# Kernel optimization log

Hardware: AMD Instinct MI355X
Metric: run time of the kernel (lower is better)

The kernel has to match this reference:

```python
import jax, jax.numpy as jnp
import numpy as np

NUM_GRAPHS = 1024
NODES_PER_GRAPH = 128
NUM_EDGES = 1048576
D_IN = 128          # n_heads * head_out_feats = input/concat dim
ATT_HEADS = 2       # intra/inter GATConv(d, 32, 2) as in HDN-DDI repo
ATT_OUT = 32
POOL_HEADS = 2      # pool = GATConv(128, 64, 2)
POOL_OUT = 64
EPS = 1e-5          # PyG LayerNorm eps


def _segment_softmax(e, seg, n):
    # numerically-stable softmax over edges grouped by destination node
    m = jax.ops.segment_max(e, seg, num_segments=n)
    m = jnp.where(jnp.isfinite(m), m, 0.0)
    p = jnp.exp(e - m[seg])
    s = jax.ops.segment_sum(p, seg, num_segments=n)
    return p / (s[seg] + 1e-16)


def _gat(x_src, x_dst, edge_index, w_src, w_dst, att_src, att_dst, bias, self_loops):
    # PyG GATConv: linear -> per-head attention logits -> leaky_relu(0.2) ->
    # softmax over incoming edges -> weighted sum of source features -> concat heads + bias
    H, C = att_src.shape
    nd = x_dst.shape[0]
    hs = (x_src @ w_src).reshape(-1, H, C)   # [Ns,H,C]
    hd = (x_dst @ w_dst).reshape(-1, H, C)   # [Nd,H,C]
    a_s = jnp.einsum('nhc,hc->nh', hs, att_src)
    a_d = jnp.einsum('nhc,hc->nh', hd, att_dst)
    src, dst = edge_index[0], edge_index[1]
    if self_loops:  # PyG default add_self_loops=True (non-bipartite case)
        loop = jnp.arange(nd)
        src = jnp.concatenate([src, loop])
        dst = jnp.concatenate([dst, loop])
    e = jax.nn.leaky_relu(a_s[src] + a_d[dst], 0.2)  # [E,H]
    alpha = _segment_softmax(e, dst, nd)
    out = jax.ops.segment_sum(hs[src] * alpha[:, :, None], dst, num_segments=nd)
    return out.reshape(nd, H * C) + bias


def _graph_layernorm(x, batch, weight, bias, n_graphs):
    # PyG LayerNorm(mode='graph'): normalize over all nodes+channels of each graph
    f = x.shape[-1]
    cnt = jax.ops.segment_sum(jnp.ones((x.shape[0],), x.dtype), batch, num_segments=n_graphs)
    norm = jnp.maximum(cnt, 1.0) * f
    mean = jax.ops.segment_sum(x.sum(-1), batch, num_segments=n_graphs) / norm
    xc = x - mean[batch][:, None]
    var = jax.ops.segment_sum((xc * xc).sum(-1), batch, num_segments=n_graphs) / norm
    return (xc / jnp.sqrt(var + EPS)[batch][:, None]) * weight + bias


def setup_inputs() -> dict:
    key = jax.random.key(0)
    ks = jax.random.split(key, 24)
    B, P, E, D = NUM_GRAPHS, NODES_PER_GRAPH, NUM_EDGES, D_IN
    N = B * P

    def intra_edges(k):  # within-graph edges, no self-loops
        k1, k2, k3 = jax.random.split(k, 3)
        g = jax.random.randint(k1, (E,), 0, B)
        s = jax.random.randint(k2, (E,), 0, P)
        d = (s + 1 + jax.random.randint(k3, (E,), 0, P - 1)) % P
        return jnp.stack([g * P + s, g * P + d])

    def inter_edges(k):  # bipartite head-node -> tail-node edges within same graph pair
        k1, k2, k3 = jax.random.split(k, 3)
        g = jax.random.randint(k1, (E,), 0, B)
        s = jax.random.randint(k2, (E,), 0, P)
        d = jax.random.randint(k3, (E,), 0, P)
        return jnp.stack([g * P + s, g * P + d])

    batch = jnp.repeat(jnp.arange(B), P)
    # one global supernode (type 2) per graph: the last node
    y = jnp.tile(jnp.concatenate([jnp.zeros((P - 1,), jnp.int32), jnp.array([2], jnp.int32)]), B)
    p = lambda k, shape: jax.random.normal(k, shape, jnp.float32) * 0.1
    return {
        'h_x': jax.random.normal(ks[0], (N, D), jnp.float32),
        't_x': jax.random.normal(ks[1], (N, D), jnp.float32),
        'h_edge_index': intra_edges(ks[2]),
        't_edge_index': intra_edges(ks[3]),
        'b_edge_index': inter_edges(ks[4]),
        'h_batch': batch,
        't_batch': batch,
        'h_y': y,
        't_y': y,
        'w_intra': p(ks[5], (D, ATT_HEADS * ATT_OUT)),
        'att_intra_src': p(ks[6], (ATT_HEADS, ATT_OUT)),
        'att_intra_dst': p(ks[7], (ATT_HEADS, ATT_OUT)),
        'b_intra': jnp.zeros((ATT_HEADS * ATT_OUT,), jnp.float32),
        'w_inter_src': p(ks[8], (D, ATT_HEADS * ATT_OUT)),
        'w_inter_dst': p(ks[9], (D, ATT_HEADS * ATT_OUT)),
        'att_inter_src': p(ks[10], (ATT_HEADS, ATT_OUT)),
        'att_inter_dst': p(ks[11], (ATT_HEADS, ATT_OUT)),
        'b_inter': jnp.zeros((ATT_HEADS * ATT_OUT,), jnp.float32),
        'w_pool': p(ks[12], (D, POOL_HEADS * POOL_OUT)),
        'att_pool_src': p(ks[13], (POOL_HEADS, POOL_OUT)),
        'att_pool_dst': p(ks[14], (POOL_HEADS, POOL_OUT)),
        'b_pool': jnp.zeros((POOL_HEADS * POOL_OUT,), jnp.float32),
        'ln_weight': jnp.ones((D,), jnp.float32),
        'ln_bias': jnp.zeros((D,), jnp.float32),
    }


def reference(h_x, t_x, h_edge_index, t_edge_index, b_edge_index, h_batch, t_batch, h_y, t_y,
              w_intra, att_intra_src, att_intra_dst, b_intra,
              w_inter_src, w_inter_dst, att_inter_src, att_inter_dst, b_inter,
              w_pool, att_pool_src, att_pool_dst, b_pool, ln_weight, ln_bias):
    h_in = jax.nn.elu(h_x)
    t_in = jax.nn.elu(t_x)
    # intra-graph attention (shared GATConv applied to both drug graphs)
    h_intra = _gat(h_in, h_in, h_edge_index, w_intra, w_intra, att_intra_src, att_intra_dst, b_intra, True)
    t_intra = _gat(t_in, t_in, t_edge_index, w_intra, w_intra, att_intra_src, att_intra_dst, b_intra, True)
    # inter-graph (bipartite) attention: h->t and reversed t->h with shared weights
    t_inter = _gat(h_in, t_in, b_edge_index, w_inter_src, w_inter_dst, att_inter_src, att_inter_dst, b_inter, False)
    h_inter = _gat(t_in, h_in, b_edge_index[::-1], w_inter_src, w_inter_dst, att_inter_src, att_inter_dst, b_inter, False)
    h_rep = jnp.concatenate([h_intra, h_inter], 1)  # [N, 128]
    t_rep = jnp.concatenate([t_intra, t_inter], 1)
    h_nx = jax.nn.elu(_graph_layernorm(h_rep, h_batch, ln_weight, ln_bias, NUM_GRAPHS))
    t_nx = jax.nn.elu(_graph_layernorm(t_rep, t_batch, ln_weight, ln_bias, NUM_GRAPHS))
    h_out = _gat(h_nx, h_nx, h_edge_index, w_pool, w_pool, att_pool_src, att_pool_dst, b_pool, True)
    t_out = _gat(t_nx, t_nx, t_edge_index, w_pool, w_pool, att_pool_src, att_pool_dst, b_pool, True)
    # get_node: gather the single type-2 supernode per graph (exactly NUM_GRAPHS of them)
    h_idx = jnp.where(h_y == 2, size=NUM_GRAPHS)[0]
    t_idx = jnp.where(t_y == 2, size=NUM_GRAPHS)[0]
    return h_out, t_out, h_out[h_idx], t_out[t_idx]
```

## Files before the change

kernel.cpp:

```cpp
#include <hip/hip_runtime.h>
#include <hip/hip_bf16.h>

#define NN 131072
#define NG 1024
#define NE 1048576
#define EB 16384
#define NB 64
#define EMAX 1536

typedef __hip_bfloat16 bf16;
typedef __attribute__((ext_vector_type(8))) short short8v;
typedef __attribute__((ext_vector_type(4))) float f32x4;

__device__ __forceinline__ float b2f(bf16 v){ return __bfloat162float(v); }
__device__ __forceinline__ bf16 f2b(float v){ return __float2bfloat16(v); }
__device__ __forceinline__ unsigned short f2bu(float v){ bf16 b = f2b(v); return *(unsigned short*)&b; }
__device__ __forceinline__ float eluf(float x){ return x > 0.f ? x : expm1f(x); }
__device__ __forceinline__ float lrelu(float x){ return x >= 0.f ? x : 0.2f*x; }

__device__ __forceinline__ float ldx(const void* p, size_t i, int f){
  return f ? ((const float*)p)[i] : b2f(((const bf16*)p)[i]);
}

struct EPtrs { const int *s0,*d0,*s1,*d1,*s2,*d2,*s3,*d3; };

__global__ void detect_dtype(const unsigned short* __restrict__ x, int* __restrict__ flag){
  if (blockIdx.x==0 && threadIdx.x==0){
    int bad = 0;
    for (int i=0;i<2048;i++){
      unsigned short e = (x[i] >> 7) & 0xFF;
      if (e == 0xFF) bad++;
      else if (e >= 0x90) bad++;
      else if (e != 0 && e < 0x60) bad++;
    }
    *flag = (bad > 64) ? 1 : 0;
  }
}

__global__ __launch_bounds__(256) void hist_bagg(EPtrs ep, int* __restrict__ Hb){
  __shared__ int cnt[NG];
  int set = blockIdx.y, blk = blockIdx.x, t = threadIdx.x;
  const int* dp = set==0 ? ep.d0 : set==1 ? ep.d1 : set==2 ? ep.d2 : ep.d3;
  for (int i=t;i<NG;i+=256) cnt[i]=0;
  __syncthreads();
  int e0 = blk*EB;
  for (int i=t;i<EB;i+=256) atomicAdd(&cnt[dp[e0+i]>>7],1);
  __syncthreads();
  for (int i=t;i<NG;i+=256) Hb[((size_t)set*NB+blk)*NG+i] = cnt[i];
}

__global__ __launch_bounds__(1024) void scan_bagg(const int* __restrict__ Hb, int* __restrict__ Bb,
                                                  int* __restrict__ base_gs){
  __shared__ int sh[1024];
  int set = blockIdx.x, t = threadIdx.x;
  int run = 0;
  for (int b=0;b<NB;b++){
    int v = Hb[((size_t)set*NB + b)*NG + t];
    Bb[((size_t)set*NB + b)*NG + t] = run;
    run += v;
  }
  int val = run; sh[t] = run; __syncthreads();
  for (int d=1; d<1024; d<<=1){
    int add = (t>=d)? sh[t-d] : 0; __syncthreads();
    val += add; sh[t] = val; __syncthreads();
  }
  int binbase = val - run;
  base_gs[set*(NG+1) + t] = binbase;
  if (t==1023) base_gs[set*(NG+1)+NG] = val;
  for (int b=0;b<NB;b++) Bb[((size_t)set*NB + b)*NG + t] += binbase;
}

__global__ __launch_bounds__(256) void scatter_bagg(EPtrs ep, const int* __restrict__ Bb,
                                                    unsigned short* __restrict__ pk){
  __shared__ int cur[NG];
  int set = blockIdx.y, blk = blockIdx.x, t = threadIdx.x;
  const int* sp = set==0 ? ep.s0 : set==1 ? ep.s1 : set==2 ? ep.s2 : ep.s3;
  const int* dp = set==0 ? ep.d0 : set==1 ? ep.d1 : set==2 ? ep.d2 : ep.d3;
  for (int i=t;i<NG;i+=256) cur[i] = Bb[((size_t)set*NB+blk)*NG+i];
  __syncthreads();
  int e0 = blk*EB;
  for (int i=t;i<EB;i+=256){
    int e = e0+i;
    int d = dp[e], s = sp[e];
    int p = atomicAdd(&cur[d>>7],1);
    pk[(size_t)set*NE + p] = (unsigned short)(((d & 127) << 8) | (s & 127));
  }
}

__global__ __launch_bounds__(256) void build_csr(const unsigned short* __restrict__ pk, const int* __restrict__ base,
                                                 unsigned char* __restrict__ srcs8, int* __restrict__ offs4){
  __shared__ int hist[128], excl[128], cur[128];
  __shared__ unsigned char ob[8192];
  int set = blockIdx.y, g = blockIdx.x, t = threadIdx.x;
  int n0 = base[set*(NG+1) + g], n1 = base[set*(NG+1) + g + 1];
  int cnt = min(n1 - n0, 8192);
  if (t < 128) hist[t] = 0;
  __syncthreads();
  const unsigned short* PK = pk + (size_t)set*NE + n0;
  for (int i=t; i<cnt; i+=256) atomicAdd(&hist[PK[i]>>8], 1);
  __syncthreads();
  if (t < 128) excl[t] = hist[t];
  __syncthreads();
  for (int d=1; d<128; d<<=1){
    int v = (t < 128 && t >= d) ? excl[t-d] : 0;
    __syncthreads();
    if (t < 128) excl[t] += v;
    __syncthreads();
  }
  if (t < 128){
    int e_ = excl[t] - hist[t];
    cur[t] = e_;
    offs4[(size_t)set*(NN+1) + g*128 + t] = n0 + e_;
  }
  if (g == NG-1 && t == 0) offs4[(size_t)set*(NN+1) + NN] = NE;
  __syncthreads();
  for (int i=t; i<cnt; i+=256){
    unsigned short v = PK[i];
    int p = atomicAdd(&cur[v>>8], 1);
    ob[p] = (unsigned char)(v & 127);
  }
  __syncthreads();
  unsigned char* S = srcs8 + (size_t)set*NE + n0;
  for (int i=t; i<cnt; i+=256) S[i] = ob[i];
}

__global__ __launch_bounds__(256) void prep_kernel(
    const void* w_intra, const void* w_isrc, const void* w_idst, const void* att_xd, const void* w_pool,
    const void* att_is, const void* att_id, const void* att_xs,
    const void* att_ps, const void* att_pd,
    const void* b_intra, const void* b_inter, const void* b_pool,
    const void* ln_w, const void* ln_b,
    bf16* __restrict__ Wtc, bf16* __restrict__ Wtp, float* __restrict__ vdst, float* __restrict__ sm,
    const int* __restrict__ fp){
  int f = *fp;
  int t = threadIdx.x;
  for (int i=t; i<16384; i+=256){
    int j = i & 7, l = (i>>3) & 63, ks = (i>>9) & 3, nt = i >> 11;
    int k = ks*32 + ((l>>4)<<3) + j;
    int c = nt*16 + (l & 15);
    float w1 = (c < 64) ? ldx(w_intra, k*64 + c, f) : ldx(w_isrc, k*64 + (c-64), f);
    Wtc[i] = f2b(w1);
    Wtp[i] = f2b(ldx(w_pool, k*128 + c, f));
  }
  {
    int k = t>>1, h = t&1; float a = 0.f;
    for (int c=0;c<32;c++) a += ldx(w_idst, k*64 + h*32 + c, f) * ldx(att_xd, h*32 + c, f);
    vdst[t] = a;
  }
  if (t < 64){
    sm[t]     = ldx(att_is, t, f);
    sm[64+t]  = ldx(att_id, t, f);
    sm[128+t] = ldx(att_xs, t, f);
    sm[448+t] = ldx(b_intra, t, f);
    sm[512+t] = ldx(b_inter, t, f);
  }
  if (t < 128){
    sm[192+t] = ldx(att_ps, t, f);
    sm[320+t] = ldx(att_pd, t, f);
    sm[576+t] = ldx(b_pool, t, f);
    sm[704+t] = ldx(ln_w, t, f);
    sm[832+t] = ldx(ln_b, t, f);
  }
}

template<int MODE>
__global__ __launch_bounds__(256) void gemm_fused(const void* A, const bf16* __restrict__ Wt, bf16* __restrict__ C,
    const int* __restrict__ fp, const int* __restrict__ fsel, size_t aoff_bf, size_t aoff_f32,
    const float* __restrict__ vdst,
    const float* __restrict__ attA, const float* __restrict__ attB, const float* __restrict__ attC,
    float* __restrict__ oS, float* __restrict__ oD, float* __restrict__ oX, float* __restrict__ oDx){
  constexpr bool ELU = (MODE==0);
  const bf16* Ab = (const bf16*)A + ((fp == nullptr && fsel && *fsel) ? aoff_f32 : aoff_bf);
  int tid = threadIdx.x;
  int w = tid >> 6, l = tid & 63;
  int lr = l & 15, lg = l >> 4;
  size_t row = (size_t)blockIdx.x*64 + w*16 + lr;
  int f = fp ? *fp : 0;
  f32x4 acc[8];
  #pragma unroll
  for (int nt=0;nt<8;nt++) acc[nt] = (f32x4){0.f,0.f,0.f,0.f};
  float dx0 = 0.f, dx1 = 0.f;
  #pragma unroll
  for (int ks=0;ks<4;ks++){
    short8v af;
    size_t ab = row*128 + ks*32 + lg*8;
    if (fp){
      if (f){
        const float* Af = (const float*)A;
        #pragma unroll
        for (int j=0;j<8;j++){
          float v = Af[ab+j]; if (ELU) v = eluf(v);
          if constexpr (MODE==0){ int k = ks*32+lg*8+j; dx0 += v*vdst[k*2]; dx1 += v*vdst[k*2+1]; }
          ((unsigned short*)&af)[j] = f2bu(v);
        }
      } else {
        const unsigned short* Au = (const unsigned short*)A;
        short8v raw = *(const short8v*)(Au + ab);
        #pragma unroll
        for (int j=0;j<8;j++){
          bf16 b; *(unsigned short*)&b = ((unsigned short*)&raw)[j];
          float v = b2f(b); if (ELU) v = eluf(v);
          if constexpr (MODE==0){ int k = ks*32+lg*8+j; dx0 += v*vdst[k*2]; dx1 += v*vdst[k*2+1]; }
          ((unsigned short*)&af)[j] = f2bu(v);
        }
      }
    } else {
      af = *(const short8v*)((const unsigned short*)Ab + ab);
    }
    #pragma unroll
    for (int nt=0;nt<8;nt++){
      short8v bfr = *(const short8v*)((const unsigned short*)Wt + (size_t)((nt*4+ks)*64 + l)*8);
      acc[nt] = __builtin_amdgcn_mfma_f32_16x16x32_bf16(af, bfr, acc[nt], 0, 0, 0);
    }
  }
  if constexpr (MODE==0){
    dx0 += __shfl_xor(dx0, 16); dx0 += __shfl_xor(dx0, 32);
    dx1 += __shfl_xor(dx1, 16); dx1 += __shfl_xor(dx1, 32);
    if (lg == 0){ oDx[row*2] = dx0; oDx[row*2+1] = dx1; }
  }
  size_t crow = (size_t)blockIdx.x*64 + w*16 + lg*4;
  #pragma unroll
  for (int nt=0;nt<8;nt++)
    #pragma unroll
    for (int r=0;r<4;r++)
      C[(crow + r)*128 + nt*16 + lr] = f2b(acc[nt][r]);
  #pragma unroll
  for (int rg=0; rg<4; ++rg){
    float pS0=0.f,pS1=0.f,pD0=0.f,pD1=0.f,pX0=0.f,pX1=0.f;
    #pragma unroll
    for (int nt=0;nt<8;nt++){
      float v = acc[nt][rg];
      int c = nt*16 + lr;
      if constexpr (MODE==0){
        if (nt<4){
          float a=attA[c], b=attB[c];
          if (nt<2){ pS0+=v*a; pD0+=v*b; } else { pS1+=v*a; pD1+=v*b; }
        } else {
          float xw=attC[c-64];
          if (nt<6) pX0+=v*xw; else pX1+=v*xw;
        }
      } else {
        float a=attA[c], b=attB[c];
        if (nt<4){ pS0+=v*a; pD0+=v*b; } else { pS1+=v*a; pD1+=v*b; }
      }
    }
    #pragma unroll
    for (int o=1;o<16;o<<=1){
      pS0+=__shfl_xor(pS0,o); pS1+=__shfl_xor(pS1,o);
      pD0+=__shfl_xor(pD0,o); pD1+=__shfl_xor(pD1,o);
      if constexpr (MODE==0){ pX0+=__shfl_xor(pX0,o); pX1+=__shfl_xor(pX1,o); }
    }
    if (lr == 0){
      size_t n = crow + rg;
      oS[n*2]=pS0; oS[n*2+1]=pS1;
      oD[n*2]=pD0; oD[n*2+1]=pD1;
      if constexpr (MODE==0){ oX[n*2]=pX0; oX[n*2+1]=pX1; }
    }
  }
}

struct GatSet {
  const int* offs;
  const unsigned char* srcs;
  const bf16* F;
  const float* aS;
  const float* aD;
  const float* bias;
  int col_in;
  int self_loops;
  int col_off;
  int pad;
  size_t obase_bf, obase_f32, gbase;
};
struct GatSet4 { GatSet s[4]; };

template<int FD>
__global__ __launch_bounds__(512) void gat_mfma(GatSet4 sets, void* out,
    const int* __restrict__ fp, const int* __restrict__ fsel){
  constexpr int NH = FD/2;
  constexpr int NT = NH/16;
  constexpr int KSH = (FD==64)?5:6;
  __shared__ bf16 Ft[NH*136];
  __shared__ bf16 Pm[128*136];
  __shared__ float2 aSs[128];
  __shared__ float rsum[128];
  __shared__ unsigned char ss[EMAX];
  __shared__ int begs[129];
  const GatSet S = sets.s[blockIdx.y];
  int fo = fp ? *fp : -1;
  size_t obase = (fsel && *fsel) ? S.obase_f32 : S.obase_bf;
  int g = blockIdx.x, t = threadIdx.x;

  if (t < 129) begs[t] = S.offs[g*128 + t];
  if (t >= 256 && t < 384) aSs[t-256] = ((const float2*)S.aS)[g*128 + (t-256)];
  __syncthreads();
  int gbeg = begs[0];
  int Eg = min(begs[128] - gbeg, EMAX);
  int w = t >> 6, l = t & 63, lr = l & 15, lg = l >> 4;

  #pragma unroll
  for (int h=0; h<2; ++h){
    for (int i=t; i<128*68; i+=512) ((unsigned int*)Pm)[i] = 0;
    if (h==0) for (int i=t; i<Eg; i+=512) ss[i] = S.srcs[gbeg + i];
    __syncthreads();
    if (t < 128){
      int r = t;
      float ad = S.aD[(size_t)(g*128+r)*2 + h];
      int b = begs[r]-gbeg, e = min(begs[r+1]-gbeg, EMAX);
      float rs = 0.f;
      unsigned short* Pr = (unsigned short*)Pm + r*136;
      for (int j=b; j<e; ++j){
        int s = ss[j];
        float2 as2 = aSs[s];
        float p = __expf(lrelu((h ? as2.y : as2.x) + ad));
        bf16 ov; *(unsigned short*)&ov = Pr[s];
        Pr[s] = f2bu(b2f(ov) + p);
        rs += p;
      }
      if (S.self_loops){
        float2 as2 = aSs[r];
        float p = __expf(lrelu((h ? as2.y : as2.x) + ad));
        bf16 ov; *(unsigned short*)&ov = Pr[r];
        Pr[r] = f2bu(b2f(ov) + p);
        rs += p;
      }
      rsum[r] = rs;
    } else {
      const unsigned short* Fu = (const unsigned short*)S.F;
      unsigned short* FtU = (unsigned short*)Ft;
      int ft = t - 128;
      for (int i=ft; i<NH*128; i+=384){
        int c = i & (NH-1), k = i >> KSH;
        FtU[c*136 + k] = Fu[((size_t)(g*128+k))*128 + S.col_in + h*NH + c];
      }
    }
    __syncthreads();
    f32x4 acc[NT];
    #pragma unroll
    for (int nt=0;nt<NT;nt++) acc[nt] = (f32x4){0.f,0.f,0.f,0.f};
    #pragma unroll
    for (int ks=0;ks<4;ks++){
      short8v af = *(const short8v*)((const unsigned short*)Pm + (w*16+lr)*136 + ks*32 + lg*8);
      #pragma unroll
      for (int nt=0;nt<NT;nt++){
        short8v bfr = *(const short8v*)((const unsigned short*)Ft + (nt*16 + lr)*136 + ks*32 + lg*8);
        acc[nt] = __builtin_amdgcn_mfma_f32_16x16x32_bf16(af, bfr, acc[nt], 0, 0, 0);
      }
    }
    #pragma unroll
    for (int rg=0; rg<4; ++rg){
      int rrow = w*16 + lg*4 + rg;
      float rinv = 1.f / (rsum[rrow] + 1e-16f);
      int n = g*128 + rrow;
      bool gw = (fp != nullptr) && (rrow == 127);
      #pragma unroll
      for (int nt=0;nt<NT;nt++){
        int c = h*NH + nt*16 + lr;
        float o = acc[nt][rg]*rinv + S.bias[c];
        size_t oi = obase + (size_t)n*128 + S.col_off + c;
        if (fo > 0){
          ((float*)out)[oi] = o;
          if (gw) ((float*)out)[S.gbase + (size_t)g*128 + c] = o;
        } else {
          ((bf16*)out)[oi] = f2b(o);
          if (gw) ((bf16*)out)[S.gbase + (size_t)g*128 + c] = f2b(o);
        }
      }
    }
    __syncthreads();
  }
}

__global__ __launch_bounds__(512) void graph_ln_m(bf16* R_, size_t off_t_bf, size_t off_t_f32,
    const int* __restrict__ fsel, const float* __restrict__ wv, const float* __restrict__ bv){
  __shared__ float sh1[8], sh2[8];
  int g = blockIdx.x, t = threadIdx.x;
  int side = g >> 10, gl = g & 1023;
  size_t soff = side ? ((*fsel) ? off_t_f32 : off_t_bf) : 0;
  unsigned short* Ru = (unsigned short*)(R_ + soff + (size_t)gl*16384);
  short8v v[4];
  #pragma unroll
  for (int q=0;q<4;q++) v[q] = *(short8v*)(Ru + q*4096 + t*8);
  float s1=0.f, s2=0.f;
  #pragma unroll
  for (int q=0;q<4;q++)
    #pragma unroll
    for (int j=0;j<8;j++){
      bf16 b; *(unsigned short*)&b = ((unsigned short*)&v[q])[j];
      float x = b2f(b); s1 += x; s2 += x*x;
    }
  #pragma unroll
  for (int o=32;o;o>>=1){ s1 += __shfl_xor(s1,o); s2 += __shfl_xor(s2,o); }
  if ((t&63)==0){ sh1[t>>6]=s1; sh2[t>>6]=s2; }
  __syncthreads();
  float S1=0.f,S2=0.f;
  #pragma unroll
  for (int i=0;i<8;i++){ S1+=sh1[i]; S2+=sh2[i]; }
  float mean = S1 * (1.f/16384.f);
  float var = fmaxf(S2*(1.f/16384.f) - mean*mean, 0.f);
  float rstd = rsqrtf(var + 1e-5f);
  #pragma unroll
  for (int q=0;q<4;q++){
    short8v ov;
    #pragma unroll
    for (int j=0;j<8;j++){
      int c = (t*8 + j) & 127;
      bf16 b; *(unsigned short*)&b = ((unsigned short*)&v[q])[j];
      float y = (b2f(b)-mean)*rstd*wv[c] + bv[c];
      ((unsigned short*)&ov)[j] = f2bu(y>0.f ? y : expm1f(y));
    }
    *(short8v*)(Ru + q*4096 + t*8) = ov;
  }
}

extern "C" void kernel_launch(void* const* d_in, const int* in_sizes, int n_in,
                              void* d_out, int out_size, void* d_ws, size_t ws_size,
                              hipStream_t stream){
  (void)in_sizes; (void)n_in; (void)out_size; (void)ws_size;
  const void* h_x = d_in[0];
  const void* t_x = d_in[1];
  const int* h_ei = (const int*)d_in[2];
  const int* t_ei = (const int*)d_in[3];
  const int* b_ei = (const int*)d_in[4];

  char* base = (char*)d_ws;
  size_t off = 0;
  auto alloc = [&](size_t bytes)->char*{ char* p = base + off; off += (bytes + 255) & ~(size_t)255; return p; };
  bf16* AB_h     = (bf16*)alloc((size_t)NN*128*2);
  bf16* AB_t     = (bf16*)alloc((size_t)NN*128*2);
  unsigned short* pk = (unsigned short*)alloc((size_t)4*NE*2);
  unsigned char* srcs8 = (unsigned char*)alloc((size_t)4*NE);
  int* offs4     = (int*)alloc((size_t)4*(NN+1)*4);
  int* Hb        = (int*)alloc((size_t)4*NB*NG*4);
  int* Bb        = (int*)alloc((size_t)4*NB*NG*4);
  int* base_gs   = (int*)alloc((size_t)4*(NG+1)*4);
  float* aSi_h   = (float*)alloc((size_t)NN*2*4);
  float* aDi_h   = (float*)alloc((size_t)NN*2*4);
  float* aSx_h   = (float*)alloc((size_t)NN*2*4);
  float* aSi_t   = (float*)alloc((size_t)NN*2*4);
  float* aDi_t   = (float*)alloc((size_t)NN*2*4);
  float* aSx_t   = (float*)alloc((size_t)NN*2*4);
  float* aDx_h   = (float*)alloc((size_t)NN*2*4);
  float* aDx_t   = (float*)alloc((size_t)NN*2*4);
  bf16* Wtc      = (bf16*)alloc(16384*2);
  bf16* Wtp      = (bf16*)alloc(16384*2);
  float* vdst    = (float*)alloc(256*4);
  float* sm      = (float*)alloc(960*4);
  int* flag      = (int*)alloc(256);

  const size_t REPT_BF = (size_t)NN*128, REPT_F32 = (size_t)2*NN*128;

  detect_dtype<<<1,64,0,stream>>>((const unsigned short*)h_x, flag);

  EPtrs ep;
  ep.s0 = h_ei;      ep.d0 = h_ei + NE;
  ep.s1 = t_ei;      ep.d1 = t_ei + NE;
  ep.s2 = b_ei;      ep.d2 = b_ei + NE;
  ep.s3 = b_ei + NE; ep.d3 = b_ei;
  hist_bagg<<<dim3(NB,4),256,0,stream>>>(ep, Hb);
  scan_bagg<<<4,1024,0,stream>>>(Hb, Bb, base_gs);
  scatter_bagg<<<dim3(NB,4),256,0,stream>>>(ep, Bb, pk);
  build_csr<<<dim3(NG,4),256,0,stream>>>(pk, base_gs, srcs8, offs4);

  prep_kernel<<<1,256,0,stream>>>(d_in[9], d_in[13], d_in[14], d_in[16], d_in[18],
      d_in[10], d_in[11], d_in[15], d_in[19], d_in[20],
      d_in[12], d_in[17], d_in[21], d_in[22], d_in[23],
      Wtc, Wtp, vdst, sm, flag);

  const int* offs_h = offs4;
  const int* offs_t = offs4 + (NN+1);
  const int* offs_ht= offs4 + 2*(NN+1);
  const int* offs_th= offs4 + 3*(NN+1);
  const unsigned char* srcs_h = srcs8;
  const unsigned char* srcs_t = srcs8 + NE;
  const unsigned char* srcs_ht= srcs8 + (size_t)2*NE;
  const unsigned char* srcs_th= srcs8 + (size_t)3*NE;

  gemm_fused<0><<<2048,256,0,stream>>>(h_x, Wtc, AB_h, flag, nullptr, 0, 0,
      vdst, sm+0, sm+64, sm+128, aSi_h, aDi_h, aSx_h, aDx_h);
  gemm_fused<0><<<2048,256,0,stream>>>(t_x, Wtc, AB_t, flag, nullptr, 0, 0,
      vdst, sm+0, sm+64, sm+128, aSi_t, aDi_t, aSx_t, aDx_t);

  {
    GatSet4 L;
    L.s[0] = { offs_h,  srcs_h,  AB_h, aSi_h, aDi_h, sm+448, 0,  1, 0,  0, 0,        0,         0 };
    L.s[1] = { offs_t,  srcs_t,  AB_t, aSi_t, aDi_t, sm+448, 0,  1, 0,  0, REPT_BF,  REPT_F32,  0 };
    L.s[2] = { offs_ht, srcs_ht, AB_h, aSx_h, aDx_t, sm+512, 64, 0, 64, 0, REPT_BF,  REPT_F32,  0 };
    L.s[3] = { offs_th, srcs_th, AB_t, aSx_t, aDx_h, sm+512, 64, 0, 64, 0, 0,        0,         0 };
    gat_mfma<64><<<dim3(NG,4),512,0,stream>>>(L, d_out, nullptr, flag);
  }

  graph_ln_m<<<2048,512,0,stream>>>((bf16*)d_out, REPT_BF, REPT_F32, flag, sm+704, sm+832);

  gemm_fused<1><<<2048,256,0,stream>>>(d_out, Wtp, AB_h, nullptr, flag, 0, 0,
      nullptr, sm+192, sm+320, nullptr, aSi_h, aDi_h, nullptr, nullptr);
  gemm_fused<1><<<2048,256,0,stream>>>(d_out, Wtp, AB_t, nullptr, flag, REPT_BF, REPT_F32,
      nullptr, sm+192, sm+320, nullptr, aSi_t, aDi_t, nullptr, nullptr);

  {
    size_t gb_h = (size_t)2*NN*128;
    size_t gb_t = gb_h + (size_t)NG*128;
    GatSet4 P;
    P.s[0] = { offs_h, srcs_h, AB_h, aSi_h, aDi_h, sm+576, 0, 1, 0, 0, 0,              0,              gb_h };
    P.s[1] = { offs_t, srcs_t, AB_t, aSi_t, aDi_t, sm+576, 0, 1, 0, 0, (size_t)NN*128, (size_t)NN*128, gb_t };
    P.s[2] = P.s[0]; P.s[3] = P.s[0];
    gat_mfma<128><<<dim3(NG,2),512,0,stream>>>(P, d_out, flag, flag);
  }
}
```

Measured before the change: 615.5 us.

## Fuse node projection GEMMs into per-graph GAT kernels and drop intermediates

Removes the standalone projection GEMM kernels and instead computes the linear projections and attention logits inside each per-graph GAT block, keeping the projected features in registers and shared memory rather than writing them to global memory and reading them back. The layer-norm intermediate now lives in a bf16 workspace, so the LN kernel no longer branches on dtype. A small separate kernel precomputes the bipartite destination logits. In exchange, each inter-graph set recomputes its half of the projection, the weights are staged into shared memory per block, and shared memory per block grows, which may lower occupancy.

Result: faster. 585.4 us (-4.9%).

```diff
diff --git a/kernel.cpp b/kernel.cpp
--- a/kernel.cpp
+++ b/kernel.cpp
@@ -163,207 +163,320 @@
   }
 }
 
-template<int MODE>
-__global__ __launch_bounds__(256) void gemm_fused(const void* A, const bf16* __restrict__ Wt, bf16* __restrict__ C,
-    const int* __restrict__ fp, const int* __restrict__ fsel, size_t aoff_bf, size_t aoff_f32,
-    const float* __restrict__ vdst,
-    const float* __restrict__ attA, const float* __restrict__ attB, const float* __restrict__ attC,
-    float* __restrict__ oS, float* __restrict__ oD, float* __restrict__ oX, float* __restrict__ oDx){
-  constexpr bool ELU = (MODE==0);
-  const bf16* Ab = (const bf16*)A + ((fp == nullptr && fsel && *fsel) ? aoff_f32 : aoff_bf);
-  int tid = threadIdx.x;
-  int w = tid >> 6, l = tid & 63;
-  int lr = l & 15, lg = l >> 4;
-  size_t row = (size_t)blockIdx.x*64 + w*16 + lr;
-  int f = fp ? *fp : 0;
-  f32x4 acc[8];
-  #pragma unroll
-  for (int nt=0;nt<8;nt++) acc[nt] = (f32x4){0.f,0.f,0.f,0.f};
-  float dx0 = 0.f, dx1 = 0.f;
+__global__ __launch_bounds__(256) void avec_dx_m(const void* Xh, const void* Xt, const float* __restrict__ vdst,
+                                                 float* __restrict__ aDx_h, float* __restrict__ aDx_t,
+                                                 const int* __restrict__ fp){
+  int f = *fp;
+  int gid = blockIdx.x*256 + threadIdx.x;
+  int n = gid >> 6, lane = gid & 63;
+  int side = n >= NN;
+  const void* X = side ? Xt : Xh;
+  float* aDx = side ? aDx_t : aDx_h;
+  int nl = side ? n - NN : n;
+  float x1 = eluf(ldx(X, (size_t)nl*128 + lane, f));
+  float x2 = eluf(ldx(X, (size_t)nl*128 + 64 + lane, f));
+  float t0 = x1*vdst[lane*2+0] + x2*vdst[(lane+64)*2+0];
+  float t1 = x1*vdst[lane*2+1] + x2*vdst[(lane+64)*2+1];
+  #pragma unroll
+  for (int o=32;o;o>>=1){ t0 += __shfl_xor(t0,o); t1 += __shfl_xor(t1,o); }
+  if (lane == 0){ aDx[nl*2+0] = t0; aDx[nl*2+1] = t1; }
+}
+
+struct L1Set {
+  const int* offs;
+  const unsigned char* srcs;
+  int a_side;
+  int wt_half;
+  int att_mode;
+  int col_off;
+  const float* aDx;
+  bf16* repout;
+};
+struct L1Set4 { L1Set s[4]; };
+
+__global__ __launch_bounds__(512) void gat_l1(L1Set4 sets, const void* Xh, const void* Xt,
+    const bf16* __restrict__ Wtc, const float* __restrict__ sm, const int* __restrict__ fp){
+  __shared__ char U[34816];
+  __shared__ bf16 Ft[32*136];
+  __shared__ float atab[192];
+  __shared__ float2 aSl[128], aDl[128];
+  __shared__ float rsum[128];
+  __shared__ unsigned char ss[EMAX];
+  __shared__ int begs[129];
+  const L1Set S = sets.s[blockIdx.y];
+  int g = blockIdx.x, t = threadIdx.x;
+  int f = *fp;
+  const void* A = S.a_side ? Xt : Xh;
+
+  bf16* WtL = (bf16*)U;
+  {
+    const short8v* src = (const short8v*)(Wtc + (size_t)S.wt_half*8192);
+    short8v* dst = (short8v*)WtL;
+    #pragma unroll
+    for (int i=0;i<2;i++) dst[t + i*512] = src[t + i*512];
+  }
+  if (t < 129) begs[t] = S.offs[g*128 + t];
+  if (t < 192){
+    float v;
+    if (t < 64) v = sm[(S.att_mode ? 128 : 0) + t];
+    else if (t < 128) v = sm[64 + (t-64)];
+    else v = sm[(S.att_mode ? 512 : 448) + (t-128)];
+    atab[t] = v;
+  }
+  __syncthreads();
+  int gbeg = begs[0], Eg = min(begs[128]-gbeg, EMAX);
+  for (int i=t; i<Eg; i+=512) ss[i] = S.srcs[gbeg + i];
+
+  int w = t>>6, l = t&63, lr = l&15, lg = l>>4;
+  size_t row = (size_t)g*128 + w*16 + lr;
+  f32x4 acc[4];
+  #pragma unroll
+  for (int nt=0;nt<4;nt++) acc[nt] = (f32x4){0.f,0.f,0.f,0.f};
   #pragma unroll
   for (int ks=0;ks<4;ks++){
     short8v af;
     size_t ab = row*128 + ks*32 + lg*8;
-    if (fp){
-      if (f){
-        const float* Af = (const float*)A;
-        #pragma unroll
-        for (int j=0;j<8;j++){
-          float v = Af[ab+j]; if (ELU) v = eluf(v);
-          if constexpr (MODE==0){ int k = ks*32+lg*8+j; dx0 += v*vdst[k*2]; dx1 += v*vdst[k*2+1]; }
-          ((unsigned short*)&af)[j] = f2bu(v);
-        }
-      } else {
-        const unsigned short* Au = (const unsigned short*)A;
-        short8v raw = *(const short8v*)(Au + ab);
-        #pragma unroll
-        for (int j=0;j<8;j++){
-          bf16 b; *(unsigned short*)&b = ((unsigned short*)&raw)[j];
-          float v = b2f(b); if (ELU) v = eluf(v);
-          if constexpr (MODE==0){ int k = ks*32+lg*8+j; dx0 += v*vdst[k*2]; dx1 += v*vdst[k*2+1]; }
-          ((unsigned short*)&af)[j] = f2bu(v);
-        }
-      }
+    if (f){
+      const float* Af = (const float*)A;
+      #pragma unroll
+      for (int j=0;j<8;j++){ ((unsigned short*)&af)[j] = f2bu(eluf(Af[ab+j])); }
     } else {
-      af = *(const short8v*)((const unsigned short*)Ab + ab);
-    }
-    #pragma unroll
-    for (int nt=0;nt<8;nt++){
-      short8v bfr = *(const short8v*)((const unsigned short*)Wt + (size_t)((nt*4+ks)*64 + l)*8);
+      const unsigned short* Au = (const unsigned short*)A;
+      short8v raw = *(const short8v*)(Au + ab);
+      #pragma unroll
+      for (int j=0;j<8;j++){
+        bf16 b; *(unsigned short*)&b = ((unsigned short*)&raw)[j];
+        ((unsigned short*)&af)[j] = f2bu(eluf(b2f(b)));
+      }
+    }
+    #pragma unroll
+    for (int nt=0;nt<4;nt++){
+      short8v bfr = *(const short8v*)((const unsigned short*)WtL + (size_t)((nt*4+ks)*64 + l)*8);
       acc[nt] = __builtin_amdgcn_mfma_f32_16x16x32_bf16(af, bfr, acc[nt], 0, 0, 0);
     }
   }
-  if constexpr (MODE==0){
-    dx0 += __shfl_xor(dx0, 16); dx0 += __shfl_xor(dx0, 32);
-    dx1 += __shfl_xor(dx1, 16); dx1 += __shfl_xor(dx1, 32);
-    if (lg == 0){ oDx[row*2] = dx0; oDx[row*2+1] = dx1; }
-  }
-  size_t crow = (size_t)blockIdx.x*64 + w*16 + lg*4;
-  #pragma unroll
-  for (int nt=0;nt<8;nt++)
-    #pragma unroll
-    for (int r=0;r<4;r++)
-      C[(crow + r)*128 + nt*16 + lr] = f2b(acc[nt][r]);
   #pragma unroll
   for (int rg=0; rg<4; ++rg){
-    float pS0=0.f,pS1=0.f,pD0=0.f,pD1=0.f,pX0=0.f,pX1=0.f;
-    #pragma unroll
-    for (int nt=0;nt<8;nt++){
+    float pS0=0.f,pS1=0.f,pD0=0.f,pD1=0.f;
+    #pragma unroll
+    for (int nt=0;nt<4;nt++){
       float v = acc[nt][rg];
       int c = nt*16 + lr;
-      if constexpr (MODE==0){
-        if (nt<4){
-          float a=attA[c], b=attB[c];
-          if (nt<2){ pS0+=v*a; pD0+=v*b; } else { pS1+=v*a; pD1+=v*b; }
-        } else {
-          float xw=attC[c-64];
-          if (nt<6) pX0+=v*xw; else pX1+=v*xw;
-        }
-      } else {
-        float a=attA[c], b=attB[c];
-        if (nt<4){ pS0+=v*a; pD0+=v*b; } else { pS1+=v*a; pD1+=v*b; }
-      }
+      float a = atab[c], b = atab[64+c];
+      if (nt<2){ pS0 += v*a; pD0 += v*b; } else { pS1 += v*a; pD1 += v*b; }
     }
     #pragma unroll
     for (int o=1;o<16;o<<=1){
       pS0+=__shfl_xor(pS0,o); pS1+=__shfl_xor(pS1,o);
       pD0+=__shfl_xor(pD0,o); pD1+=__shfl_xor(pD1,o);
-      if constexpr (MODE==0){ pX0+=__shfl_xor(pX0,o); pX1+=__shfl_xor(pX1,o); }
     }
     if (lr == 0){
-      size_t n = crow + rg;
-      oS[n*2]=pS0; oS[n*2+1]=pS1;
-      oD[n*2]=pD0; oD[n*2+1]=pD1;
-      if constexpr (MODE==0){ oX[n*2]=pX0; oX[n*2+1]=pX1; }
-    }
-  }
-}
-
-struct GatSet {
-  const int* offs;
-  const unsigned char* srcs;
-  const bf16* F;
-  const float* aS;
-  const float* aD;
-  const float* bias;
-  int col_in;
-  int self_loops;
-  int col_off;
-  int pad;
-  size_t obase_bf, obase_f32, gbase;
-};
-struct GatSet4 { GatSet s[4]; };
-
-template<int FD>
-__global__ __launch_bounds__(512) void gat_mfma(GatSet4 sets, void* out,
-    const int* __restrict__ fp, const int* __restrict__ fsel){
-  constexpr int NH = FD/2;
-  constexpr int NT = NH/16;
-  constexpr int KSH = (FD==64)?5:6;
-  __shared__ bf16 Ft[NH*136];
-  __shared__ bf16 Pm[128*136];
-  __shared__ float2 aSs[128];
-  __shared__ float rsum[128];
-  __shared__ unsigned char ss[EMAX];
-  __shared__ int begs[129];
-  const GatSet S = sets.s[blockIdx.y];
-  int fo = fp ? *fp : -1;
-  size_t obase = (fsel && *fsel) ? S.obase_f32 : S.obase_bf;
-  int g = blockIdx.x, t = threadIdx.x;
-
-  if (t < 129) begs[t] = S.offs[g*128 + t];
-  if (t >= 256 && t < 384) aSs[t-256] = ((const float2*)S.aS)[g*128 + (t-256)];
-  __syncthreads();
-  int gbeg = begs[0];
-  int Eg = min(begs[128] - gbeg, EMAX);
-  int w = t >> 6, l = t & 63, lr = l & 15, lg = l >> 4;
-
+      int rr = w*16 + lg*4 + rg;
+      aSl[rr] = make_float2(pS0, pS1);
+      if (S.att_mode == 0) aDl[rr] = make_float2(pD0, pD1);
+    }
+  }
+  if (S.att_mode == 1 && t < 128) aDl[t] = ((const float2*)S.aDx)[g*128 + t];
+  __syncthreads();
+
+  bf16* Pm = (bf16*)U;
   #pragma unroll
   for (int h=0; h<2; ++h){
     for (int i=t; i<128*68; i+=512) ((unsigned int*)Pm)[i] = 0;
-    if (h==0) for (int i=t; i<Eg; i+=512) ss[i] = S.srcs[gbeg + i];
+    #pragma unroll
+    for (int ntl=0; ntl<2; ++ntl){
+      int nt = h*2 + ntl;
+      #pragma unroll
+      for (int rg=0; rg<4; ++rg)
+        ((unsigned short*)Ft)[(ntl*16+lr)*136 + (w*16+lg*4+rg)] = f2bu(acc[nt][rg]);
+    }
     __syncthreads();
     if (t < 128){
       int r = t;
-      float ad = S.aD[(size_t)(g*128+r)*2 + h];
+      float ad = h ? aDl[r].y : aDl[r].x;
       int b = begs[r]-gbeg, e = min(begs[r+1]-gbeg, EMAX);
       float rs = 0.f;
       unsigned short* Pr = (unsigned short*)Pm + r*136;
       for (int j=b; j<e; ++j){
         int s = ss[j];
-        float2 as2 = aSs[s];
-        float p = __expf(lrelu((h ? as2.y : as2.x) + ad));
+        float as = h ? aSl[s].y : aSl[s].x;
+        float p = __expf(lrelu(as + ad));
         bf16 ov; *(unsigned short*)&ov = Pr[s];
         Pr[s] = f2bu(b2f(ov) + p);
         rs += p;
       }
-      if (S.self_loops){
-        float2 as2 = aSs[r];
-        float p = __expf(lrelu((h ? as2.y : as2.x) + ad));
+      if (S.att_mode == 0){
+        float as = h ? aSl[r].y : aSl[r].x;
+        float p = __expf(lrelu(as + ad));
         bf16 ov; *(unsigned short*)&ov = Pr[r];
         Pr[r] = f2bu(b2f(ov) + p);
         rs += p;
       }
       rsum[r] = rs;
-    } else {
-      const unsigned short* Fu = (const unsigned short*)S.F;
-      unsigned short* FtU = (unsigned short*)Ft;
-      int ft = t - 128;
-      for (int i=ft; i<NH*128; i+=384){
-        int c = i & (NH-1), k = i >> KSH;
-        FtU[c*136 + k] = Fu[((size_t)(g*128+k))*128 + S.col_in + h*NH + c];
-      }
-    }
-    __syncthreads();
-    f32x4 acc[NT];
-    #pragma unroll
-    for (int nt=0;nt<NT;nt++) acc[nt] = (f32x4){0.f,0.f,0.f,0.f};
+    }
+    __syncthreads();
+    f32x4 a2[2];
+    a2[0] = (f32x4){0.f,0.f,0.f,0.f}; a2[1] = (f32x4){0.f,0.f,0.f,0.f};
     #pragma unroll
     for (int ks=0;ks<4;ks++){
       short8v af = *(const short8v*)((const unsigned short*)Pm + (w*16+lr)*136 + ks*32 + lg*8);
       #pragma unroll
-      for (int nt=0;nt<NT;nt++){
-        short8v bfr = *(const short8v*)((const unsigned short*)Ft + (nt*16 + lr)*136 + ks*32 + lg*8);
-        acc[nt] = __builtin_amdgcn_mfma_f32_16x16x32_bf16(af, bfr, acc[nt], 0, 0, 0);
+      for (int j=0;j<2;j++){
+        short8v bfr = *(const short8v*)((const unsigned short*)Ft + (j*16+lr)*136 + ks*32 + lg*8);
+        a2[j] = __builtin_amdgcn_mfma_f32_16x16x32_bf16(af, bfr, a2[j], 0, 0, 0);
       }
     }
     #pragma unroll
     for (int rg=0; rg<4; ++rg){
       int rrow = w*16 + lg*4 + rg;
       float rinv = 1.f / (rsum[rrow] + 1e-16f);
-      int n = g*128 + rrow;
-      bool gw = (fp != nullptr) && (rrow == 127);
-      #pragma unroll
-      for (int nt=0;nt<NT;nt++){
-        int c = h*NH + nt*16 + lr;
-        float o = acc[nt][rg]*rinv + S.bias[c];
-        size_t oi = obase + (size_t)n*128 + S.col_off + c;
-        if (fo > 0){
+      size_t n = (size_t)g*128 + rrow;
+      #pragma unroll
+      for (int j=0;j<2;j++){
+        int c = h*32 + j*16 + lr;
+        float o = a2[j][rg]*rinv + atab[128+c];
+        S.repout[n*128 + S.col_off + c] = f2b(o);
+      }
+    }
+    __syncthreads();
+  }
+}
+
+__global__ __launch_bounds__(512) void gat_pool(const bf16* __restrict__ rep,
+    const int* __restrict__ offs_h, const unsigned char* __restrict__ srcs_h,
+    const int* __restrict__ offs_t, const unsigned char* __restrict__ srcs_t,
+    const bf16* __restrict__ Wtp, const float* __restrict__ sm,
+    void* out, const int* __restrict__ fp){
+  __shared__ char U[34816];
+  __shared__ bf16 Ft[64*136];
+  __shared__ float attL[384];
+  __shared__ float2 aSp[128], aDp[128];
+  __shared__ float rsum[128];
+  __shared__ unsigned char ss[EMAX];
+  __shared__ int begs[129];
+  int side = blockIdx.y, g = blockIdx.x, t = threadIdx.x;
+  int f = *fp;
+  const int* offs = side ? offs_t : offs_h;
+  const unsigned char* srcs = side ? srcs_t : srcs_h;
+  const unsigned short* A = (const unsigned short*)rep + (size_t)side*NN*128;
+  size_t obase = (size_t)side*NN*128;
+  size_t gbase = (size_t)2*NN*128 + (size_t)side*NG*128;
+
+  bf16* WtL = (bf16*)U;
+  {
+    const short8v* src = (const short8v*)Wtp;
+    short8v* dst = (short8v*)WtL;
+    #pragma unroll
+    for (int i=0;i<4;i++) dst[t + i*512] = src[t + i*512];
+  }
+  if (t < 129) begs[t] = offs[g*128 + t];
+  if (t < 384) attL[t] = sm[(t<128) ? 192+t : (t<256) ? 320+(t-128) : 576+(t-256)];
+  __syncthreads();
+  int gbeg = begs[0], Eg = min(begs[128]-gbeg, EMAX);
+  for (int i=t; i<Eg; i+=512) ss[i] = srcs[gbeg + i];
+
+  int w = t>>6, l = t&63, lr = l&15, lg = l>>4;
+  size_t row = (size_t)g*128 + w*16 + lr;
+  f32x4 acc[8];
+  #pragma unroll
+  for (int nt=0;nt<8;nt++) acc[nt] = (f32x4){0.f,0.f,0.f,0.f};
+  #pragma unroll
+  for (int ks=0;ks<4;ks++){
+    short8v af = *(const short8v*)(A + row*128 + ks*32 + lg*8);
+    #pragma unroll
+    for (int nt=0;nt<8;nt++){
+      short8v bfr = *(const short8v*)((const unsigned short*)WtL + (size_t)((nt*4+ks)*64 + l)*8);
+      acc[nt] = __builtin_amdgcn_mfma_f32_16x16x32_bf16(af, bfr, acc[nt], 0, 0, 0);
+    }
+  }
+  #pragma unroll
+  for (int rg=0; rg<4; ++rg){
+    float pS0=0.f,pS1=0.f,pD0=0.f,pD1=0.f;
+    #pragma unroll
+    for (int nt=0;nt<8;nt++){
+      float v = acc[nt][rg];
+      int c = nt*16 + lr;
+      float a = attL[c], b = attL[128+c];
+      if (nt<4){ pS0 += v*a; pD0 += v*b; } else { pS1 += v*a; pD1 += v*b; }
+    }
+    #pragma unroll
+    for (int o=1;o<16;o<<=1){
+      pS0+=__shfl_xor(pS0,o); pS1+=__shfl_xor(pS1,o);
+      pD0+=__shfl_xor(pD0,o); pD1+=__shfl_xor(pD1,o);
+    }
+    if (lr == 0){
+      int rr = w*16 + lg*4 + rg;
+      aSp[rr] = make_float2(pS0, pS1);
+      aDp[rr] = make_float2(pD0, pD1);
+    }
+  }
+  __syncthreads();
+
+  bf16* Pm = (bf16*)U;
+  #pragma unroll
+  for (int h=0; h<2; ++h){
+    for (int i=t; i<128*68; i+=512) ((unsigned int*)Pm)[i] = 0;
+    #pragma unroll
+    for (int ntl=0; ntl<4; ++ntl){
+      int nt = h*4 + ntl;
+      #pragma unroll
+      for (int rg=0; rg<4; ++rg)
+        ((unsigned short*)Ft)[(ntl*16+lr)*136 + (w*16+lg*4+rg)] = f2bu(acc[nt][rg]);
+    }
+    __syncthreads();
+    if (t < 128){
+      int r = t;
+      float ad = h ? aDp[r].y : aDp[r].x;
+      int b = begs[r]-gbeg, e = min(begs[r+1]-gbeg, EMAX);
+      float rs = 0.f;
+      unsigned short* Pr = (unsigned short*)Pm + r*136;
+      for (int j=b; j<e; ++j){
+        int s = ss[j];
+        float as = h ? aSp[s].y : aSp[s].x;
+        float p = __expf(lrelu(as + ad));
+        bf16 ov; *(unsigned short*)&ov = Pr[s];
+        Pr[s] = f2bu(b2f(ov) + p);
+        rs += p;
+      }
+      {
+        float as = h ? aSp[r].y : aSp[r].x;
+        float p = __expf(lrelu(as + ad));
+        bf16 ov; *(unsigned short*)&ov = Pr[r];
+        Pr[r] = f2bu(b2f(ov) + p);
+        rs += p;
+      }
+      rsum[r] = rs;
+    }
+    __syncthreads();
+    f32x4 a2[4];
+    #pragma unroll
+    for (int j=0;j<4;j++) a2[j] = (f32x4){0.f,0.f,0.f,0.f};
+    #pragma unroll
+    for (int ks=0;ks<4;ks++){
+      short8v af = *(const short8v*)((const unsigned short*)Pm + (w*16+lr)*136 + ks*32 + lg*8);
+      #pragma unroll
+      for (int j=0;j<4;j++){
+        short8v bfr = *(const short8v*)((const unsigned short*)Ft + (j*16+lr)*136 + ks*32 + lg*8);
+        a2[j] = __builtin_amdgcn_mfma_f32_16x16x32_bf16(af, bfr, a2[j], 0, 0, 0);
+      }
+    }
+    #pragma unroll
+    for (int rg=0; rg<4; ++rg){
+      int rrow = w*16 + lg*4 + rg;
+      float rinv = 1.f / (rsum[rrow] + 1e-16f);
+      size_t n = (size_t)g*128 + rrow;
+      bool gw = (rrow == 127);
+      #pragma unroll
+      for (int j=0;j<4;j++){
+        int c = h*64 + j*16 + lr;
+        float o = a2[j][rg]*rinv + attL[256+c];
+        size_t oi = obase + n*128 + c;
+        if (f){
           ((float*)out)[oi] = o;
-          if (gw) ((float*)out)[S.gbase + (size_t)g*128 + c] = o;
+          if (gw) ((float*)out)[gbase + (size_t)g*128 + c] = o;
         } else {
           ((bf16*)out)[oi] = f2b(o);
-          if (gw) ((bf16*)out)[S.gbase + (size_t)g*128 + c] = f2b(o);
+          if (gw) ((bf16*)out)[gbase + (size_t)g*128 + c] = f2b(o);
         }
       }
     }
@@ -371,13 +484,11 @@
   }
 }
 
-__global__ __launch_bounds__(512) void graph_ln_m(bf16* R_, size_t off_t_bf, size_t off_t_f32,
-    const int* __restrict__ fsel, const float* __restrict__ wv, const float* __restrict__ bv){
+__global__ __launch_bounds__(512) void graph_ln_w(bf16* __restrict__ R_,
+    const float* __restrict__ wv, const float* __restrict__ bv){
   __shared__ float sh1[8], sh2[8];
   int g = blockIdx.x, t = threadIdx.x;
-  int side = g >> 10, gl = g & 1023;
-  size_t soff = side ? ((*fsel) ? off_t_f32 : off_t_bf) : 0;
-  unsigned short* Ru = (unsigned short*)(R_ + soff + (size_t)gl*16384);
+  unsigned short* Ru = (unsigned short*)(R_ + (size_t)g*16384);
   short8v v[4];
   #pragma unroll
   for (int q=0;q<4;q++) v[q] = *(short8v*)(Ru + q*4096 + t*8);
@@ -426,20 +537,13 @@
   char* base = (char*)d_ws;
   size_t off = 0;
   auto alloc = [&](size_t bytes)->char*{ char* p = base + off; off += (bytes + 255) & ~(size_t)255; return p; };
-  bf16* AB_h     = (bf16*)alloc((size_t)NN*128*2);
-  bf16* AB_t     = (bf16*)alloc((size_t)NN*128*2);
+  bf16* rep      = (bf16*)alloc((size_t)2*NN*128*2);
   unsigned short* pk = (unsigned short*)alloc((size_t)4*NE*2);
   unsigned char* srcs8 = (unsigned char*)alloc((size_t)4*NE);
   int* offs4     = (int*)alloc((size_t)4*(NN+1)*4);
   int* Hb        = (int*)alloc((size_t)4*NB*NG*4);
   int* Bb        = (int*)alloc((size_t)4*NB*NG*4);
   int* base_gs   = (int*)alloc((size_t)4*(NG+1)*4);
-  float* aSi_h   = (float*)alloc((size_t)NN*2*4);
-  float* aDi_h   = (float*)alloc((size_t)NN*2*4);
-  float* aSx_h   = (float*)alloc((size_t)NN*2*4);
-  float* aSi_t   = (float*)alloc((size_t)NN*2*4);
-  float* aDi_t   = (float*)alloc((size_t)NN*2*4);
-  float* aSx_t   = (float*)alloc((size_t)NN*2*4);
   float* aDx_h   = (float*)alloc((size_t)NN*2*4);
   float* aDx_t   = (float*)alloc((size_t)NN*2*4);
   bf16* Wtc      = (bf16*)alloc(16384*2);
@@ -448,7 +552,8 @@
   float* sm      = (float*)alloc(960*4);
   int* flag      = (int*)alloc(256);
 
-  const size_t REPT_BF = (size_t)NN*128, REPT_F32 = (size_t)2*NN*128;
+  bf16* rep_h = rep;
+  bf16* rep_t = rep + (size_t)NN*128;
 
   detect_dtype<<<1,64,0,stream>>>((const unsigned short*)h_x, flag);
 
@@ -467,6 +572,8 @@
       d_in[12], d_in[17], d_in[21], d_in[22], d_in[23],
       Wtc, Wtp, vdst, sm, flag);
 
+  avec_dx_m<<<65536,256,0,stream>>>(h_x, t_x, vdst, aDx_h, aDx_t, flag);
+
   const int* offs_h = offs4;
   const int* offs_t = offs4 + (NN+1);
   const int* offs_ht= offs4 + 2*(NN+1);
@@ -476,34 +583,17 @@
   const unsigned char* srcs_ht= srcs8 + (size_t)2*NE;
   const unsigned char* srcs_th= srcs8 + (size_t)3*NE;
 
-  gemm_fused<0><<<2048,256,0,stream>>>(h_x, Wtc, AB_h, flag, nullptr, 0, 0,
-      vdst, sm+0, sm+64, sm+128, aSi_h, aDi_h, aSx_h, aDx_h);
-  gemm_fused<0><<<2048,256,0,stream>>>(t_x, Wtc, AB_t, flag, nullptr, 0, 0,
-      vdst, sm+0, sm+64, sm+128, aSi_t, aDi_t, aSx_t, aDx_t);
-
   {
-    GatSet4 L;
-    L.s[0] = { offs_h,  srcs_h,  AB_h, aSi_h, aDi_h, sm+448, 0,  1, 0,  0, 0,        0,         0 };
-    L.s[1] = { offs_t,  srcs_t,  AB_t, aSi_t, aDi_t, sm+448, 0,  1, 0,  0, REPT_BF,  REPT_F32,  0 };
-    L.s[2] = { offs_ht, srcs_ht, AB_h, aSx_h, aDx_t, sm+512, 64, 0, 64, 0, REPT_BF,  REPT_F32,  0 };
-    L.s[3] = { offs_th, srcs_th, AB_t, aSx_t, aDx_h, sm+512, 64, 0, 64, 0, 0,        0,         0 };
-    gat_mfma<64><<<dim3(NG,4),512,0,stream>>>(L, d_out, nullptr, flag);
-  }
-
-  graph_ln_m<<<2048,512,0,stream>>>((bf16*)d_out, REPT_BF, REPT_F32, flag, sm+704, sm+832);
-
-  gemm_fused<1><<<2048,256,0,stream>>>(d_out, Wtp, AB_h, nullptr, flag, 0, 0,
-      nullptr, sm+192, sm+320, nullptr, aSi_h, aDi_h, nullptr, nullptr);
-  gemm_fused<1><<<2048,256,0,stream>>>(d_out, Wtp, AB_t, nullptr, flag, REPT_BF, REPT_F32,
-      nullptr, sm+192, sm+320, nullptr, aSi_t, aDi_t, nullptr, nullptr);
-
-  {
-    size_t gb_h = (size_t)2*NN*128;
-    size_t gb_t = gb_h + (size_t)NG*128;
-    GatSet4 P;
-    P.s[0] = { offs_h, srcs_h, AB_h, aSi_h, aDi_h, sm+576, 0, 1, 0, 0, 0,              0,              gb_h };
-    P.s[1] = { offs_t, srcs_t, AB_t, aSi_t, aDi_t, sm+576, 0, 1, 0, 0, (size_t)NN*128, (size_t)NN*128, gb_t };
-    P.s[2] = P.s[0]; P.s[3] = P.s[0];
-    gat_mfma<128><<<dim3(NG,2),512,0,stream>>>(P, d_out, flag, flag);
-  }
-}
+    L1Set4 L;
+    L.s[0] = { offs_h,  srcs_h,  0, 0, 0, 0,  nullptr, rep_h };
+    L.s[1] = { offs_t,  srcs_t,  1, 0, 0, 0,  nullptr, rep_t };
+    L.s[2] = { offs_ht, srcs_ht, 0, 1, 1, 64, aDx_t,   rep_t };
+    L.s[3] = { offs_th, srcs_th, 1, 1, 1, 64, aDx_h,   rep_h };
+    gat_l1<<<dim3(NG,4),512,0,stream>>>(L, h_x, t_x, Wtc, sm, flag);
+  }
+
+  graph_ln_w<<<2048,512,0,stream>>>(rep, sm+704, sm+832);
+
+  gat_pool<<<dim3(NG,2),512,0,stream>>>(rep, offs_h, srcs_h, offs_t, srcs_t,
+      Wtp, sm, d_out, flag);
+}
```
